# Kernel optimization log

Measured on AMD Instinct MI355X. Metric: run time of the kernel, lower is better.

The kernel has to match this reference:

```python
import jax, jax.numpy as jnp
import numpy as np

N = 128                      # reduced state dimension (Q_dim[0])
S = N * (N + 1) // 2         # number of triu pairwise products = 8256
BATCH = 16384                # snapshot columns
_rows, _cols = np.triu_indices(N)
ROWS = jnp.asarray(_rows)    # [S] int32 constants
COLS = jnp.asarray(_cols)


def setup_inputs() -> dict:
    key = jax.random.key(0)
    kx, ka, kb = jax.random.split(key, 3)
    x = jax.random.normal(kx, (N, BATCH), dtype=jnp.float32)
    # learned operators (module inits them to zeros; use small random for a meaningful baseline)
    A = jax.random.normal(ka, (N, N), dtype=jnp.float32) * 0.02
    B = jax.random.normal(kb, (N, S), dtype=jnp.float32) * 0.02
    return {"x": x, "A": A, "B": B}


def reference(x, A, B):
    # quadratic feature expansion: x2[k, :] = x[i_k, :] * x[j_k, :] over triu pairs
    x2 = x[ROWS] * x[COLS]                 # [S, BATCH]
    return A @ x + B @ x2                  # [N, BATCH]
```

## Files before the change

kernel.cpp:

```cpp
#include <hip/hip_runtime.h>


constexpr int N_     = 128;
constexpr int S_     = 8256;
constexpr int BATCH_ = 16384;
constexpr int KTOT   = 8384;
constexpr int NKT    = 131;
constexpr int LD     = 136;
constexpr size_t WT_BYTES = (size_t)KTOT * 128 * 2;
constexpr size_t PP_OFF   = WT_BYTES;

typedef __attribute__((ext_vector_type(8))) short short8;
typedef __attribute__((ext_vector_type(4))) float f32x4;
typedef __attribute__((ext_vector_type(2))) float f32x2;

__device__ __forceinline__ float bf2f(ushort h) {
    unsigned u = (unsigned)h << 16;
    float f;
    __builtin_memcpy(&f, &u, 4);
    return f;
}
__device__ __forceinline__ ushort f2bf(float f) {
    unsigned u;
    __builtin_memcpy(&u, &f, 4);
    u = (u + 0x7FFFu + ((u >> 16) & 1u)) >> 16;
    return (ushort)u;
}
__device__ __forceinline__ uint fbits(float f) {
    uint u; __builtin_memcpy(&u, &f, 4); return u;
}

__global__ void build_perm(ushort* __restrict__ pp) {
    int i = threadIdx.x;
    if (i >= 128) return;
    pp[i] = (ushort)(i | (0xFFu << 8));
    int off_n = 0, off_r = 0;
    for (int q = 0; q < i; ++q) {
        off_n += 16 - ((q + 7) >> 3);
        off_r += (8 - (q & 7)) & 7;
    }
    const int jb0 = (i + 7) >> 3;
    const int kb = 128 + off_n * 8;
    for (int jb = jb0; jb < 16; ++jb) {
        const int j0 = jb * 8;
        for (int e = 0; e < 8; ++e)
            pp[kb + (jb - jb0) * 8 + e] = (ushort)(i | ((j0 + e) << 8));
    }
    const int h = (8 - (i & 7)) & 7;
    const int rb = 7936 + off_r;
    for (int e = 0; e < h; ++e)
        pp[rb + e] = (ushort)(i | ((i + e) << 8));
}

__global__ void build_wt(const float* __restrict__ A, const float* __restrict__ B,
                         const ushort* __restrict__ pp, ushort* __restrict__ wt) {
    int e  = blockIdx.x * 256 + threadIdx.x;
    int kt = e >> 13;
    int r  = e & 8191;
    int kk = r >> 12;
    int wmm = (r >> 11) & 1;
    int mt = (r >> 9) & 3;
    int lane = (r >> 3) & 63;
    int el = r & 7;
    int m  = wmm * 64 + mt * 16 + (lane & 15);
    int k  = kt * 64 + kk * 32 + (lane >> 4) * 8 + el;
    uint pr = pp[k];
    uint i = pr & 0xFFu, j = pr >> 8;
    float v;
    if (j == 0xFFu) v = A[m * 128 + i];
    else {
        int s = (int)(i * (257 - i) / 2 + (j - i));
        v = B[(size_t)m * S_ + s];
    }
    wt[e] = f2bf(v);
}

__device__ __forceinline__ void load_af(short8 af[8], const ushort* __restrict__ wt,
                                        int kt, int wm, int lane) {
    const ushort* ab = wt + ((size_t)kt << 13) + (wm << 11) + (lane << 3);
    #pragma unroll
    for (int kk = 0; kk < 2; ++kk)
        #pragma unroll
        for (int mt = 0; mt < 4; ++mt)
            af[kk * 4 + mt] = *(const short8*)(ab + (kk << 12) + (mt << 9));
}

__device__ __forceinline__ void step_nice(f32x4 acc[4][2], const short8 af[8],
                                          uint prc, const ushort* __restrict__ xr0,
                                          const ushort* __restrict__ xr1) {
    const uint i0a = prc & 0xFFu, j0a = (prc >> 8) & 0xFFu;
    const uint i0b = (prc >> 16) & 0xFFu, j0b = prc >> 24;
    const ushort xia0 = xr0[i0a], xia1 = xr1[i0a];
    const ushort xib0 = xr0[i0b], xib1 = xr1[i0b];
    uint wa0[4], wa1[4], wb0[4], wb1[4];
    __builtin_memcpy(wa0, xr0 + j0a, 16);
    __builtin_memcpy(wa1, xr1 + j0a, 16);
    __builtin_memcpy(wb0, xr0 + j0b, 16);
    __builtin_memcpy(wb1, xr1 + j0b, 16);

    short8 bfr[2][2];
    #pragma unroll
    for (int v = 0; v < 4; ++v) {
        const uint*  wsx = (v == 0) ? wa0 : (v == 1) ? wa1 : (v == 2) ? wb0 : wb1;
        const ushort xis = (v == 0) ? xia0 : (v == 1) ? xia1 : (v == 2) ? xib0 : xib1;
        const float xi = bf2f(xis);
        const f32x2 xi2 = {xi, xi};
        uint ow[4];
        #pragma unroll
        for (int p = 0; p < 4; ++p) {
            const uint lo = wsx[p] << 16;
            const uint hi = wsx[p] & 0xFFFF0000u;
            f32x2 a;
            { float fl, fh;
              __builtin_memcpy(&fl, &lo, 4);
              __builtin_memcpy(&fh, &hi, 4);
              a.x = fl; a.y = fh; }
            const f32x2 o = a * xi2;
            ow[p] = __builtin_amdgcn_perm(fbits(o.y), fbits(o.x),
                                          0x07060302u);
        }
        __builtin_memcpy(&bfr[v >> 1][v & 1], ow, 16);
    }
    #pragma unroll
    for (int kk = 0; kk < 2; ++kk)
        #pragma unroll
        for (int mt = 0; mt < 4; ++mt)
            #pragma unroll
            for (int nt = 0; nt < 2; ++nt)
                acc[mt][nt] = __builtin_amdgcn_mfma_f32_16x16x32_bf16(
                    af[kk * 4 + mt], bfr[kk][nt], acc[mt][nt], 0, 0, 0);
}

__global__ __launch_bounds__(512) void gemm_mfma(
    const float*  __restrict__ x,
    const ushort* __restrict__ wt,
    const ushort* __restrict__ pp,
    float* __restrict__ out)
{
    __shared__ ushort xt[128 * LD];
    __shared__ uint   ppc[NKT * 4];

    const int t    = threadIdx.x;
    const int b0   = blockIdx.x * 128;
    const int sp   = blockIdx.y;
    const int kt0  = sp ? 66 : 0;
    const int kt1  = sp ? NKT : 66;
    const int lane = t & 63;
    const int w    = t >> 6;
    const int wm   = w >> 2, wn = w & 3;
    const int l16  = lane & 15, quad = lane >> 4;

    {
        const int n = t & 127, g = t >> 7;
        #pragma unroll
        for (int c = 0; c < 4; ++c) {
            const int rb = g * 32 + c * 8;
            uint ow[4];
            #pragma unroll
            for (int p = 0; p < 4; ++p) {
                const ushort u0 = f2bf(x[(size_t)(rb + 2 * p) * BATCH_ + b0 + n]);
                const ushort u1 = f2bf(x[(size_t)(rb + 2 * p + 1) * BATCH_ + b0 + n]);
                ow[p] = (uint)u0 | ((uint)u1 << 16);
            }
            __builtin_memcpy(&xt[n * LD + rb], ow, 16);
        }
    }
    for (int idx = t; idx < NKT * 4; idx += 512) {
        const int kt = idx >> 2, q = idx & 3;
        const uint w0 = *(const uint*)(pp + kt * 64 + q * 8);
        const uint w1 = *(const uint*)(pp + kt * 64 + 32 + q * 8);
        ppc[idx] = (w0 & 0xFFFFu) | ((w1 & 0xFFFFu) << 16);
    }
    __syncthreads();

    f32x4 acc[4][2];
    #pragma unroll
    for (int mt = 0; mt < 4; ++mt)
        #pragma unroll
        for (int nt = 0; nt < 2; ++nt)
            acc[mt][nt] = (f32x4){0.f, 0.f, 0.f, 0.f};

    const ushort* xr0 = xt + (wn * 32 + l16) * LD;
    const ushort* xr1 = xr0 + 16 * LD;

    if (sp == 0) {
        for (int kt = 0; kt < 2; ++kt) {
            short8 af[8];
            load_af(af, wt, kt, wm, lane);
            short8 bfr[2][2];
            #pragma unroll
            for (int kk = 0; kk < 2; ++kk) {
                const int off = kt * 64 + kk * 32 + quad * 8;
                bfr[kk][0] = *(const short8*)(xr0 + off);
                bfr[kk][1] = *(const short8*)(xr1 + off);
            }
            #pragma unroll
            for (int kk = 0; kk < 2; ++kk)
                #pragma unroll
                for (int mt = 0; mt < 4; ++mt)
                    #pragma unroll
                    for (int nt = 0; nt < 2; ++nt)
                        acc[mt][nt] = __builtin_amdgcn_mfma_f32_16x16x32_bf16(
                            af[kk * 4 + mt], bfr[kk][nt], acc[mt][nt], 0, 0, 0);
        }
    }

    {
        const int s_ni = (kt0 > 2) ? kt0 : 2;
        const int e_ni = (kt1 < 124) ? kt1 : 124;
        int kt = s_ni;
        if (kt < e_ni) {
            short8 afA[8], afB[8];
            load_af(afA, wt, kt, wm, lane);
            uint prc = ppc[kt * 4 + quad];
            while (true) {
                {
                    const int ktn = (kt + 1 < e_ni) ? kt + 1 : kt;
                    load_af(afB, wt, ktn, wm, lane);
                    const uint prn = ppc[ktn * 4 + quad];
                    step_nice(acc, afA, prc, xr0, xr1);
                    prc = prn; ++kt;
                }
                if (kt >= e_ni) break;
                {
                    const int ktn = (kt + 1 < e_ni) ? kt + 1 : kt;
                    load_af(afA, wt, ktn, wm, lane);
                    const uint prn = ppc[ktn * 4 + quad];
                    step_nice(acc, afB, prc, xr0, xr1);
                    prc = prn; ++kt;
                }
                if (kt >= e_ni) break;
            }
        }
    }

    if (sp == 1) {
        for (int kt = 124; kt < NKT; ++kt) {
            short8 af[8];
            load_af(af, wt, kt, wm, lane);
            short8 bfr[2][2];
            #pragma unroll
            for (int kk = 0; kk < 2; ++kk) {
                const int k0 = kt * 64 + kk * 32 + quad * 8;
                const uint4 pk = *(const uint4*)(pp + k0);
                const uint pr4[4] = {pk.x, pk.y, pk.z, pk.w};
                #pragma unroll
                for (int nt = 0; nt < 2; ++nt) {
                    const ushort* xr = nt ? xr1 : xr0;
                    float prods[8];
                    #pragma unroll
                    for (int e = 0; e < 8; ++e) {
                        const uint ent = (pr4[e >> 1] >> ((e & 1) * 16)) & 0xFFFFu;
                        prods[e] = bf2f(xr[ent & 0xFFu]) * bf2f(xr[ent >> 8]);
                    }
                    uint ow[4];
                    #pragma unroll
                    for (int p = 0; p < 4; ++p)
                        ow[p] = __builtin_amdgcn_perm(fbits(prods[2 * p + 1]),
                                                      fbits(prods[2 * p]),
                                                      0x07060302u);
                    __builtin_memcpy(&bfr[kk][nt], ow, 16);
                }
            }
            #pragma unroll
            for (int kk = 0; kk < 2; ++kk)
                #pragma unroll
                for (int mt = 0; mt < 4; ++mt)
                    #pragma unroll
                    for (int nt = 0; nt < 2; ++nt)
                        acc[mt][nt] = __builtin_amdgcn_mfma_f32_16x16x32_bf16(
                            af[kk * 4 + mt], bfr[kk][nt], acc[mt][nt], 0, 0, 0);
        }
    }

    #pragma unroll
    for (int mt = 0; mt < 4; ++mt) {
        #pragma unroll
        for (int nt = 0; nt < 2; ++nt) {
            const int mbase = wm * 64 + mt * 16 + quad * 4;
            const size_t col = (size_t)b0 + wn * 32 + nt * 16 + l16;
            #pragma unroll
            for (int r = 0; r < 4; ++r)
                unsafeAtomicAdd(&out[(size_t)(mbase + r) * BATCH_ + col],
                                acc[mt][nt][r]);
        }
    }
}

extern "C" void kernel_launch(void* const* d_in, const int* in_sizes, int n_in,
                              void* d_out, int out_size, void* d_ws, size_t ws_size,
                              hipStream_t stream) {
    const float* x = (const float*)d_in[0];
    const float* A = (const float*)d_in[1];
    const float* B = (const float*)d_in[2];
    float* out = (float*)d_out;

    ushort* wt = (ushort*)d_ws;
    ushort* pp = (ushort*)((char*)d_ws + PP_OFF);

    hipMemsetAsync(out, 0, (size_t)N_ * BATCH_ * sizeof(float), stream);
    build_perm<<<1, 128, 0, stream>>>(pp);
    build_wt<<<4192, 256, 0, stream>>>(A, B, pp, wt);
    gemm_mfma<<<dim3(BATCH_ / 128, 2), 512, 0, stream>>>(x, wt, pp, out);
}
```

Measured before the change: 127.7 us.

## Fuse setup kernels into one launch and split GEMM K across four blocks

```diff
diff --git a/kernel.cpp b/kernel.cpp
--- a/kernel.cpp
+++ b/kernel.cpp
@@ -30,49 +30,92 @@
     uint u; __builtin_memcpy(&u, &f, 4); return u;
 }
 
-__global__ void build_perm(ushort* __restrict__ pp) {
-    int i = threadIdx.x;
-    if (i >= 128) return;
-    pp[i] = (ushort)(i | (0xFFu << 8));
-    int off_n = 0, off_r = 0;
-    for (int q = 0; q < i; ++q) {
-        off_n += 16 - ((q + 7) >> 3);
-        off_r += (8 - (q & 7)) & 7;
-    }
-    const int jb0 = (i + 7) >> 3;
-    const int kb = 128 + off_n * 8;
-    for (int jb = jb0; jb < 16; ++jb) {
-        const int j0 = jb * 8;
-        for (int e = 0; e < 8; ++e)
-            pp[kb + (jb - jb0) * 8 + e] = (ushort)(i | ((j0 + e) << 8));
-    }
-    const int h = (8 - (i & 7)) & 7;
-    const int rb = 7936 + off_r;
-    for (int e = 0; e < h; ++e)
-        pp[rb + e] = (ushort)(i | ((i + e) << 8));
-}
-
-__global__ void build_wt(const float* __restrict__ A, const float* __restrict__ B,
-                         const ushort* __restrict__ pp, ushort* __restrict__ wt) {
-    int e  = blockIdx.x * 256 + threadIdx.x;
-    int kt = e >> 13;
-    int r  = e & 8191;
-    int kk = r >> 12;
-    int wmm = (r >> 11) & 1;
-    int mt = (r >> 9) & 3;
-    int lane = (r >> 3) & 63;
-    int el = r & 7;
-    int m  = wmm * 64 + mt * 16 + (lane & 15);
-    int k  = kt * 64 + kk * 32 + (lane >> 4) * 8 + el;
-    uint pr = pp[k];
-    uint i = pr & 0xFFu, j = pr >> 8;
-    float v;
-    if (j == 0xFFu) v = A[m * 128 + i];
-    else {
-        int s = (int)(i * (257 - i) / 2 + (j - i));
-        v = B[(size_t)m * S_ + s];
-    }
-    wt[e] = f2bf(v);
+__device__ __forceinline__ int cumN(int i) {
+    if (i <= 0) return 0;
+    const int n = i - 1, t = n >> 3, r = n & 7;
+    return 16 * i - (4 * t * (t + 1) + r * (t + 1));
+}
+__device__ __forceinline__ int offR(int i) {
+    const int a = i >> 3, b = i & 7;
+    const int p = b ? (8 * (b - 1) - (((b - 1) * b) >> 1)) : 0;
+    return 28 * a + p;
+}
+__device__ __forceinline__ int triS(int i) { return i * (257 - i) / 2; }
+
+__global__ __launch_bounds__(256) void build_all(
+    const float* __restrict__ A, const float* __restrict__ B,
+    ushort* __restrict__ pp, ushort* __restrict__ wt,
+    float* __restrict__ out)
+{
+    const int bid = blockIdx.x, t = threadIdx.x;
+    if (bid < 524) {
+        const int idx = bid * 256 + t;
+        const int ko  = idx >> 7;
+        const int m   = idx & 127;
+        const int kt = ko >> 3, kk = (ko >> 2) & 1, oct = ko & 3;
+        const int lane = oct * 16 + (m & 15);
+        const int e0 = kt * 8192 + kk * 4096 + (m >> 6) * 2048 +
+                       ((m >> 4) & 3) * 512 + lane * 8;
+        float v[8];
+        if (ko < 16) {
+            const int i0 = ko * 8;
+            #pragma unroll
+            for (int el = 0; el < 8; ++el) v[el] = A[m * 128 + i0 + el];
+        } else if (ko < 992) {
+            const int o = ko - 16;
+            int i = 0;
+            #pragma unroll
+            for (int st = 64; st >= 1; st >>= 1) {
+                const int c = i + st;
+                if (c < 128 && cumN(c) <= o) i = c;
+            }
+            const int jb = ((i + 7) >> 3) + (o - cumN(i));
+            const int s0 = triS(i) + jb * 8 - i;
+            const float* bp = B + (size_t)m * S_ + s0;
+            #pragma unroll
+            for (int el = 0; el < 8; ++el) v[el] = bp[el];
+        } else {
+            const int kb = ko * 8 - 7936;
+            #pragma unroll
+            for (int el = 0; el < 8; ++el) {
+                const int kloc = kb + el;
+                int i = 0;
+                #pragma unroll
+                for (int st = 64; st >= 1; st >>= 1) {
+                    const int c = i + st;
+                    if (c < 128 && offR(c) <= kloc) i = c;
+                }
+                v[el] = B[(size_t)m * S_ + triS(i) + (kloc - offR(i))];
+            }
+        }
+        ushort o8[8];
+        #pragma unroll
+        for (int el = 0; el < 8; ++el) o8[el] = f2bf(v[el]);
+        __builtin_memcpy(wt + e0, o8, 16);
+    } else if (bid < 780) {
+        const int zb = bid - 524;
+        f32x4* o4 = (f32x4*)out;
+        #pragma unroll
+        for (int c = 0; c < 4; ++c)
+            o4[(size_t)zb * 2048 + c * 512 + t] = (f32x4){0.f, 0.f, 0.f, 0.f};
+    } else {
+        const int i = t;
+        if (i < 128) {
+            pp[i] = (ushort)(i | (0xFFu << 8));
+            const int jb0 = (i + 7) >> 3;
+            int kb = 128 + cumN(i) * 8;
+            for (int jb = jb0; jb < 16; ++jb) {
+                #pragma unroll
+                for (int e = 0; e < 8; ++e)
+                    pp[kb + e] = (ushort)(i | ((jb * 8 + e) << 8));
+                kb += 8;
+            }
+            const int h = (8 - (i & 7)) & 7;
+            const int rb = 7936 + offR(i);
+            for (int e = 0; e < h; ++e)
+                pp[rb + e] = (ushort)(i | ((i + e) << 8));
+        }
+    }
 }
 
 __device__ __forceinline__ void load_af(short8 af[8], const ushort* __restrict__ wt,
@@ -143,8 +186,8 @@
     const int t    = threadIdx.x;
     const int b0   = blockIdx.x * 128;
     const int sp   = blockIdx.y;
-    const int kt0  = sp ? 66 : 0;
-    const int kt1  = sp ? NKT : 66;
+    const int kt0  = sp * 33;
+    const int kt1  = (sp == 3) ? NKT : kt0 + 33;
     const int lane = t & 63;
     const int w    = t >> 6;
     const int wm   = w >> 2, wn = w & 3;
@@ -234,7 +277,7 @@
         }
     }
 
-    if (sp == 1) {
+    if (sp == 3) {
         for (int kt = 124; kt < NKT; ++kt) {
             short8 af[8];
             load_af(af, wt, kt, wm, lane);
@@ -298,8 +341,6 @@
     ushort* wt = (ushort*)d_ws;
     ushort* pp = (ushort*)((char*)d_ws + PP_OFF);
 
-    hipMemsetAsync(out, 0, (size_t)N_ * BATCH_ * sizeof(float), stream);
-    build_perm<<<1, 128, 0, stream>>>(pp);
-    build_wt<<<4192, 256, 0, stream>>>(A, B, pp, wt);
-    gemm_mfma<<<dim3(BATCH_ / 128, 2), 512, 0, stream>>>(x, wt, pp, out);
-}
+    build_all<<<781, 256, 0, stream>>>(A, B, pp, wt, out);
+    gemm_mfma<<<dim3(BATCH_ / 128, 4), 512, 0, stream>>>(x, wt, pp, out);
+}
```

Result: no change. 129.2 us (+1.2%).
